# Kernel optimization log

Measured on AMD Instinct MI355X. Metric: run time of the kernel, lower is better.

The kernel has to match this reference:

```python
import jax, jax.numpy as jnp
import numpy as np

B, T, E, H, HS, L, V = 128, 256, 384, 6, 64, 6, 78
FF = 4 * E  # 1536


def layer_norm(x, g, b, eps=1e-5):
    mu = jnp.mean(x, axis=-1, keepdims=True)
    var = jnp.mean((x - mu) ** 2, axis=-1, keepdims=True)
    return (x - mu) * jax.lax.rsqrt(var + eps) * g + b


def setup_inputs() -> dict:
    key = jax.random.key(0)
    ks = jax.random.split(key, 20)
    s = 0.02
    return {
        "context": jax.random.randint(ks[0], (B, T), 0, V),
        "tok_emb": jax.random.normal(ks[1], (V, E)) * s,
        "pos_emb": jax.random.normal(ks[2], (T, E)) * s,
        "ln1_g": jnp.ones((L, E)), "ln1_b": jnp.zeros((L, E)),
        "w_qkv": jax.random.normal(ks[3], (L, H, E, 3 * HS)) * s,  # per-head qkv, no bias
        "w_proj": jax.random.normal(ks[4], (L, E, E)) * s,
        "b_proj": jnp.zeros((L, E)),
        "ln2_g": jnp.ones((L, E)), "ln2_b": jnp.zeros((L, E)),
        "w1": jax.random.normal(ks[5], (L, E, FF)) * s, "b1": jnp.zeros((L, FF)),
        "w2": jax.random.normal(ks[6], (L, FF, E)) * s, "b2": jnp.zeros((L, E)),
        "lnf_g": jnp.ones((E,)), "lnf_b": jnp.zeros((E,)),
        "w_head": jax.random.normal(ks[7], (E, V)) * s, "b_head": jnp.zeros((V,)),
    }


def reference(context, tok_emb, pos_emb, ln1_g, ln1_b, w_qkv, w_proj, b_proj,
              ln2_g, ln2_b, w1, b1, w2, b2, lnf_g, lnf_b, w_head, b_head):
    x = tok_emb[context] + pos_emb[None, :, :]            # [B,T,E]
    causal = jnp.tril(jnp.ones((T, T), dtype=bool))       # lower-tri mask
    scale = HS ** (-0.5)
    for l in range(L):
        # multi-head attention (pre-LN), per-head qkv projection, no bias
        xn = layer_norm(x, ln1_g[l], ln1_b[l])
        qkv = jnp.einsum('bte,hef->bthf', xn, w_qkv[l])   # [B,T,H,3*HS]
        q, k, v = jnp.split(qkv, 3, axis=-1)              # each [B,T,H,HS]
        scores = jnp.einsum('bthd,bshd->bhts', q, k) * scale
        scores = jnp.where(causal, scores, -jnp.inf)
        att = jax.nn.softmax(scores, axis=-1)             # [B,H,T,T]
        o = jnp.einsum('bhts,bshd->bthd', att, v).reshape(B, T, E)
        x = x + o @ w_proj[l] + b_proj[l]
        # feed-forward (pre-LN)
        xn2 = layer_norm(x, ln2_g[l], ln2_b[l])
        x = x + jax.nn.relu(xn2 @ w1[l] + b1[l]) @ w2[l] + b2[l]
    x = layer_norm(x, lnf_g, lnf_b)
    return x @ w_head + b_head                            # [B,T,V]
```

## Files before the change

### kernel.cpp

```cpp
#include <hip/hip_runtime.h>


#define Bc 128
#define Tc 256
#define Ec 384
#define Hc 6
#define HSc 64
#define Lc 6
#define Vc 78
#define FFc 1536
#define Mc (Bc * Tc)

typedef unsigned short u16;
using bf16x8 = __attribute__((ext_vector_type(8))) short;
using f32x4 = __attribute__((ext_vector_type(4))) float;

__device__ __forceinline__ float b2f(u16 u) {
    union { float f; unsigned int i; } x;
    x.i = ((unsigned int)u) << 16;
    return x.f;
}
__device__ __forceinline__ u16 f2b(float f) {
    union { float f; unsigned int u; } x;
    x.f = f;
    unsigned int r = x.u + 0x7fffu + ((x.u >> 16) & 1u);
    return (u16)(r >> 16);
}

__device__ __forceinline__ void gload_lds16(const u16* g, u16* l) {
    __builtin_amdgcn_global_load_lds(
        (const __attribute__((address_space(1))) unsigned int*)g,
        (__attribute__((address_space(3))) unsigned int*)l, 16, 0, 0);
}

__global__ __launch_bounds__(256) void poison_kernel(
    float* __restrict__ out, int n, float val) {
    int i = blockIdx.x * 256 + threadIdx.x;
    if (i < n) out[i] = val;
}

__global__ __launch_bounds__(256) void trans_qkv_kernel(
    const float* __restrict__ in, u16* __restrict__ out) {
    int i = blockIdx.x * 256 + threadIdx.x;
    if (i >= Lc * Hc * Ec * 192) return;
    int f = i % 192;
    int r = i / 192;
    int e = r % Ec; r /= Ec;
    int h = r % Hc;
    int l = r / Hc;
    out[((size_t)l * 1152 + h * 192 + f) * Ec + e] = f2b(in[i]);
}
__global__ __launch_bounds__(256) void trans_w_kernel(
    const float* __restrict__ in, u16* __restrict__ out, int K, int N) {
    int i = blockIdx.x * 256 + threadIdx.x;
    if (i >= Lc * K * N) return;
    int n = i % N;
    int r = i / N;
    int k = r % K;
    int l = r / K;
    out[((size_t)l * N + n) * K + k] = f2b(in[i]);
}
__global__ __launch_bounds__(256) void trans_head_kernel(
    const float* __restrict__ in, u16* __restrict__ out) {
    int i = blockIdx.x * 256 + threadIdx.x;
    if (i >= Ec * Vc) return;
    int v = i % Vc, e = i / Vc;
    out[(size_t)v * Ec + e] = f2b(in[i]);
}

__global__ __launch_bounds__(256) void embed_kernel(
    const int* __restrict__ ctx, const float* __restrict__ tok,
    const float* __restrict__ pos, float* __restrict__ x) {
    int i = blockIdx.x * 256 + threadIdx.x;
    if (i >= Mc * Ec) return;
    int e = i % Ec, bt = i / Ec, t = bt % Tc;
    x[i] = tok[ctx[bt] * Ec + e] + pos[t * Ec + e];
}

__global__ __launch_bounds__(256) void ln_kernel(
    const float* __restrict__ X, u16* __restrict__ Y,
    const float* __restrict__ g, const float* __restrict__ b, int nrows) {
    int row = blockIdx.x * 4 + (threadIdx.x >> 6);
    int lane = threadIdx.x & 63;
    if (row >= nrows) return;
    const float* xr = X + (size_t)row * Ec;
    float v[6];
    float s = 0.f;
#pragma unroll
    for (int i = 0; i < 6; ++i) { v[i] = xr[lane + 64 * i]; s += v[i]; }
#pragma unroll
    for (int off = 32; off >= 1; off >>= 1) s += __shfl_xor(s, off, 64);
    float mean = s * (1.0f / Ec);
    float s2 = 0.f;
#pragma unroll
    for (int i = 0; i < 6; ++i) { float d = v[i] - mean; s2 += d * d; }
#pragma unroll
    for (int off = 32; off >= 1; off >>= 1) s2 += __shfl_xor(s2, off, 64);
    float rstd = rsqrtf(s2 * (1.0f / Ec) + 1e-5f);
    u16* yr = Y + (size_t)row * Ec;
#pragma unroll
    for (int i = 0; i < 6; ++i) {
        int e = lane + 64 * i;
        yr[e] = f2b((v[i] - mean) * rstd * g[e] + b[e]);
    }
}

template <bool RELU, bool RESID, bool OUTBF16, bool VECEPI>
__global__ __launch_bounds__(256) void mfma_gemm(
    const u16* __restrict__ A, const u16* __restrict__ Wt,
    const float* __restrict__ bias, const float* R, void* C,
    int K, int ldC, int NV) {
    constexpr bool SWAP = VECEPI && !OUTBF16;
    __shared__ __align__(16) u16 smem[128 * 128];
    u16(*As)[64] = (u16(*)[64])smem;
    u16(*Bs)[64] = (u16(*)[64])(smem + 128 * 64);
    int tid = threadIdx.x;

    int nwg = gridDim.x * gridDim.y;
    int bid = blockIdx.y * gridDim.x + blockIdx.x;
    int q = nwg >> 3, r = nwg & 7;
    int xcd = bid & 7, idx = bid >> 3;
    int swz = (xcd < r ? xcd * (q + 1) : r * (q + 1) + (xcd - r) * q) + idx;
    int bx = swz % gridDim.x, by = swz / gridDim.x;
    int m0 = by * 128, n0 = bx * 128;

    int w = tid >> 6, lane = tid & 63;
    int wm = (w >> 1) * 64, wn = (w & 1) * 64;
    int r16 = lane & 15, quad = lane >> 4;

    int lrow = lane >> 3;
    int scol = ((lane & 7) ^ lrow) * 8;
    const u16* ap[4];
    const u16* bp[4];
#pragma unroll
    for (int j = 0; j < 4; ++j) {
        int row = (w * 4 + j) * 8 + lrow;
        ap[j] = A + (size_t)(m0 + row) * K + scol;
        bp[j] = Wt + (size_t)(n0 + row) * K + scol;
    }

    f32x4 acc[4][4] = {};

    for (int k0 = 0; k0 < K; k0 += 64) {
        __syncthreads();
#pragma unroll
        for (int j = 0; j < 4; ++j) {
            gload_lds16(ap[j], &As[(w * 4 + j) * 8][0]);
            gload_lds16(bp[j], &Bs[(w * 4 + j) * 8][0]);
            ap[j] += 64;
            bp[j] += 64;
        }
        __syncthreads();
#pragma unroll
        for (int kk = 0; kk < 2; ++kk) {
            int csw = ((kk * 4 + quad) ^ (r16 & 7)) * 8;
            bf16x8 af[4], bf[4];
#pragma unroll
            for (int i = 0; i < 4; ++i) {
                af[i] = *reinterpret_cast<const bf16x8*>(
                    &As[wm + i * 16 + r16][csw]);
                bf[i] = *reinterpret_cast<const bf16x8*>(
                    &Bs[wn + i * 16 + r16][csw]);
            }
#pragma unroll
            for (int mi = 0; mi < 4; ++mi)
#pragma unroll
                for (int ni = 0; ni < 4; ++ni) {
                    if (SWAP)
                        acc[mi][ni] = __builtin_amdgcn_mfma_f32_16x16x32_bf16(
                            bf[ni], af[mi], acc[mi][ni], 0, 0, 0);
                    else
                        acc[mi][ni] = __builtin_amdgcn_mfma_f32_16x16x32_bf16(
                            af[mi], bf[ni], acc[mi][ni], 0, 0, 0);
                }
        }
    }

    if (VECEPI && OUTBF16) {
        float bv[4];
#pragma unroll
        for (int ni = 0; ni < 4; ++ni)
            bv[ni] = bias ? bias[n0 + wn + ni * 16 + r16] : 0.f;
        __syncthreads();
#pragma unroll
        for (int mi = 0; mi < 4; ++mi)
#pragma unroll
            for (int ni = 0; ni < 4; ++ni)
#pragma unroll
                for (int reg = 0; reg < 4; ++reg) {
                    int row = wm + mi * 16 + quad * 4 + reg;
                    int col = wn + ni * 16 + r16;
                    float v = acc[mi][ni][reg] + bv[ni];
                    if (RELU) v = fmaxf(v, 0.f);
                    int pc = (col >> 3) ^ (row & 15);
                    smem[row * 128 + pc * 8 + (col & 7)] = f2b(v);
                }
        __syncthreads();
        u16* cp = (u16*)C;
#pragma unroll
        for (int i = 0; i < 4; ++i) {
            int row = (tid >> 3) + 32 * i;
#pragma unroll
            for (int h = 0; h < 2; ++h) {
                int lc = (tid & 7) + 8 * h;
                int pc = lc ^ (row & 15);
                bf16x8 val = *reinterpret_cast<const bf16x8*>(
                    &smem[row * 128 + pc * 8]);
                *reinterpret_cast<bf16x8*>(
                    &cp[(size_t)(m0 + row) * ldC + n0 + lc * 8]) = val;
            }
        }
    } else if (VECEPI) {
        float* cp = (float*)C;
        f32x4 bv4[4];
#pragma unroll
        for (int ni = 0; ni < 4; ++ni) {
            int gn = n0 + wn + ni * 16 + quad * 4;
            if (bias)
                bv4[ni] = *reinterpret_cast<const f32x4*>(&bias[gn]);
            else
                bv4[ni] = f32x4{0.f, 0.f, 0.f, 0.f};
        }
#pragma unroll
        for (int mi = 0; mi < 4; ++mi) {
            int gm = m0 + wm + mi * 16 + r16;
#pragma unroll
            for (int ni = 0; ni < 4; ++ni) {
                int gn = n0 + wn + ni * 16 + quad * 4;
                size_t goff = (size_t)gm * ldC + gn;
                f32x4 v = acc[mi][ni] + bv4[ni];
                if (RELU) {
#pragma unroll
                    for (int e = 0; e < 4; ++e) v[e] = fmaxf(v[e], 0.f);
                }
                if (RESID) v += *reinterpret_cast<const f32x4*>(&R[goff]);
                *reinterpret_cast<f32x4*>(&cp[goff]) = v;
            }
        }
    } else {
#pragma unroll
        for (int mi = 0; mi < 4; ++mi)
#pragma unroll
            for (int ni = 0; ni < 4; ++ni) {
                int gn = n0 + wn + ni * 16 + r16;
                if (gn >= NV) continue;
                float bvs = bias ? bias[gn] : 0.f;
#pragma unroll
                for (int reg = 0; reg < 4; ++reg) {
                    int gm = m0 + wm + mi * 16 + quad * 4 + reg;
                    float v = acc[mi][ni][reg] + bvs;
                    if (RESID) v += R[(size_t)gm * ldC + gn];
                    if (RELU) v = fmaxf(v, 0.f);
                    if (OUTBF16)
                        ((u16*)C)[(size_t)gm * ldC + gn] = f2b(v);
                    else
                        ((float*)C)[(size_t)gm * ldC + gn] = v;
                }
            }
    }
}

__global__ __launch_bounds__(256) void attn_kernel(
    const u16* __restrict__ qkv, u16* __restrict__ o) {
    __shared__ u16 Qs[64][72];
    __shared__ u16 Ks[64][72];
    __shared__ u16 Vt[64][72];
    __shared__ u16 Ps[4][16][72];
    int tid = threadIdx.x;
    int tt = blockIdx.x, h = blockIdx.y, b = blockIdx.z;
    int w = tid >> 6, lane = tid & 63;
    int r16 = lane & 15, quad = lane >> 4;
    int t0 = tt * 64;
    const u16* base = qkv + (size_t)b * Tc * 1152 + h * 192;

    int sr = tid >> 2, sd = (tid & 3) * 16;
    {
        const u16* src = base + (size_t)(t0 + sr) * 1152 + sd;
        *reinterpret_cast<uint4*>(&Qs[sr][sd]) =
            *reinterpret_cast<const uint4*>(src);
        *reinterpret_cast<uint4*>(&Qs[sr][sd + 8]) =
            *reinterpret_cast<const uint4*>(src + 8);
    }

    float m_run[4], l_run[4];
#pragma unroll
    for (int r = 0; r < 4; ++r) { m_run[r] = -3.0e38f; l_run[r] = 0.f; }
    f32x4 acc_o[4] = {};

    for (int st = 0; st <= tt; ++st) {
        __syncthreads();
        {
            const u16* ks = base + (size_t)(st * 64 + sr) * 1152 + 64 + sd;
            *reinterpret_cast<uint4*>(&Ks[sr][sd]) =
                *reinterpret_cast<const uint4*>(ks);
            *reinterpret_cast<uint4*>(&Ks[sr][sd + 8]) =
                *reinterpret_cast<const uint4*>(ks + 8);
            const u16* vs = base + (size_t)(st * 64 + sr) * 1152 + 128 + sd;
            u16 tv[16];
            *reinterpret_cast<uint4*>(tv) = *reinterpret_cast<const uint4*>(vs);
            *reinterpret_cast<uint4*>(tv + 8) =
                *reinterpret_cast<const uint4*>(vs + 8);
#pragma unroll
            for (int j = 0; j < 16; ++j) Vt[sd + j][sr] = tv[j];
        }
        __syncthreads();

        f32x4 acc_s[4] = {};
        bf16x8 aq0 = *reinterpret_cast<const bf16x8*>(&Qs[w * 16 + r16][quad * 8]);
        bf16x8 aq1 = *reinterpret_cast<const bf16x8*>(&Qs[w * 16 + r16][32 + quad * 8]);
#pragma unroll
        for (int ni = 0; ni < 4; ++ni) {
            bf16x8 bk0 = *reinterpret_cast<const bf16x8*>(&Ks[ni * 16 + r16][quad * 8]);
            bf16x8 bk1 = *reinterpret_cast<const bf16x8*>(&Ks[ni * 16 + r16][32 + quad * 8]);
            acc_s[ni] = __builtin_amdgcn_mfma_f32_16x16x32_bf16(aq0, bk0, acc_s[ni], 0, 0, 0);
            acc_s[ni] = __builtin_amdgcn_mfma_f32_16x16x32_bf16(aq1, bk1, acc_s[ni], 0, 0, 0);
        }

        float sc[4][4];
        float mt[4] = {-3.0e38f, -3.0e38f, -3.0e38f, -3.0e38f};
#pragma unroll
        for (int ni = 0; ni < 4; ++ni)
#pragma unroll
            for (int reg = 0; reg < 4; ++reg) {
                int col = st * 64 + ni * 16 + r16;
                int row = t0 + w * 16 + quad * 4 + reg;
                float v = (col <= row) ? acc_s[ni][reg] * 0.125f : -3.0e38f;
                sc[ni][reg] = v;
                mt[reg] = fmaxf(mt[reg], v);
            }
#pragma unroll
        for (int reg = 0; reg < 4; ++reg) {
#pragma unroll
            for (int off = 1; off <= 8; off <<= 1)
                mt[reg] = fmaxf(mt[reg], __shfl_xor(mt[reg], off, 64));
        }
        float alpha[4], lt[4];
#pragma unroll
        for (int reg = 0; reg < 4; ++reg) {
            float m_new = fmaxf(m_run[reg], mt[reg]);
            alpha[reg] = __expf(m_run[reg] - m_new);
            m_run[reg] = m_new;
            lt[reg] = 0.f;
        }
#pragma unroll
        for (int ni = 0; ni < 4; ++ni)
#pragma unroll
            for (int reg = 0; reg < 4; ++reg) {
                float p = __expf(sc[ni][reg] - m_run[reg]);
                lt[reg] += p;
                Ps[w][quad * 4 + reg][ni * 16 + r16] = f2b(p);
            }
#pragma unroll
        for (int reg = 0; reg < 4; ++reg) {
#pragma unroll
            for (int off = 1; off <= 8; off <<= 1)
                lt[reg] += __shfl_xor(lt[reg], off, 64);
            l_run[reg] = l_run[reg] * alpha[reg] + lt[reg];
        }
#pragma unroll
        for (int ni = 0; ni < 4; ++ni)
#pragma unroll
            for (int reg = 0; reg < 4; ++reg) acc_o[ni][reg] *= alpha[reg];
        __syncthreads();

        bf16x8 ap0 = *reinterpret_cast<const bf16x8*>(&Ps[w][r16][quad * 8]);
        bf16x8 ap1 = *reinterpret_cast<const bf16x8*>(&Ps[w][r16][32 + quad * 8]);
#pragma unroll
        for (int ni = 0; ni < 4; ++ni) {
            bf16x8 bv0 = *reinterpret_cast<const bf16x8*>(&Vt[ni * 16 + r16][quad * 8]);
            bf16x8 bv1 = *reinterpret_cast<const bf16x8*>(&Vt[ni * 16 + r16][32 + quad * 8]);
            acc_o[ni] = __builtin_amdgcn_mfma_f32_16x16x32_bf16(ap0, bv0, acc_o[ni], 0, 0, 0);
            acc_o[ni] = __builtin_amdgcn_mfma_f32_16x16x32_bf16(ap1, bv1, acc_o[ni], 0, 0, 0);
        }
    }

    float inv[4];
#pragma unroll
    for (int reg = 0; reg < 4; ++reg) inv[reg] = 1.0f / l_run[reg];
#pragma unroll
    for (int ni = 0; ni < 4; ++ni)
#pragma unroll
        for (int reg = 0; reg < 4; ++reg) {
            int t = t0 + w * 16 + quad * 4 + reg;
            o[((size_t)b * Tc + t) * Ec + h * 64 + ni * 16 + r16] =
                f2b(acc_o[ni][reg] * inv[reg]);
        }
}

#define GRD(n) dim3(((n) + 255) / 256)

extern "C" void kernel_launch(void* const* d_in, const int* in_sizes, int n_in,
                              void* d_out, int out_size, void* d_ws, size_t ws_size,
                              hipStream_t stream) {
    const int* ctx = (const int*)d_in[0];
    const float* tok = (const float*)d_in[1];
    const float* pos = (const float*)d_in[2];
    const float* ln1g = (const float*)d_in[3];
    const float* ln1b = (const float*)d_in[4];
    const float* wqkv = (const float*)d_in[5];
    const float* wproj = (const float*)d_in[6];
    const float* bproj = (const float*)d_in[7];
    const float* ln2g = (const float*)d_in[8];
    const float* ln2b = (const float*)d_in[9];
    const float* w1 = (const float*)d_in[10];
    const float* b1 = (const float*)d_in[11];
    const float* w2 = (const float*)d_in[12];
    const float* b2 = (const float*)d_in[13];
    const float* lnfg = (const float*)d_in[14];
    const float* lnfb = (const float*)d_in[15];
    const float* whead = (const float*)d_in[16];
    const float* bhead = (const float*)d_in[17];
    float* out = (float*)d_out;

    char* ws = (char*)d_ws;
    float* x = (float*)ws;
    size_t off = (size_t)Mc * Ec * 4;
    u16* wqkvT = (u16*)(ws + off); off += (size_t)Lc * 1152 * 384 * 2;
    u16* wprojT = (u16*)(ws + off); off += (size_t)Lc * 384 * 384 * 2;
    u16* w1T = (u16*)(ws + off); off += (size_t)Lc * 1536 * 384 * 2;
    u16* w2T = (u16*)(ws + off); off += (size_t)Lc * 384 * 1536 * 2;
    u16* wheadT = (u16*)(ws + off); off += (size_t)128 * 384 * 2;
    const size_t per_b = (size_t)Tc * (Ec + 1152 + Ec + FFc) * 2;
    if (ws_size < off + per_b) {
        poison_kernel<<<GRD(out_size), 256, 0, stream>>>(out, out_size, 200.0f);
        return;
    }
    int CB = (int)((ws_size - off) / per_b);
    if (CB > Bc) CB = Bc;
    u16* xn_c = (u16*)(ws + off);
    u16* qkv_c = xn_c + (size_t)CB * Tc * Ec;
    u16* o_c = qkv_c + (size_t)CB * Tc * 1152;
    u16* ff_c = o_c + (size_t)CB * Tc * Ec;

    trans_qkv_kernel<<<GRD(Lc * Hc * Ec * 192), 256, 0, stream>>>(wqkv, wqkvT);
    trans_w_kernel<<<GRD(Lc * Ec * Ec), 256, 0, stream>>>(wproj, wprojT, Ec, Ec);
    trans_w_kernel<<<GRD(Lc * Ec * FFc), 256, 0, stream>>>(w1, w1T, Ec, FFc);
    trans_w_kernel<<<GRD(Lc * FFc * Ec), 256, 0, stream>>>(w2, w2T, FFc, Ec);
    hipMemsetAsync(wheadT, 0, (size_t)128 * 384 * 2, stream);
    trans_head_kernel<<<GRD(Ec * Vc), 256, 0, stream>>>(whead, wheadT);

    embed_kernel<<<GRD(Mc * Ec), 256, 0, stream>>>(ctx, tok, pos, x);

    for (int l = 0; l < Lc; ++l) {
        for (int b0 = 0; b0 < Bc; b0 += CB) {
            int bcnt = (Bc - b0 < CB) ? (Bc - b0) : CB;
            int rows = bcnt * Tc;
            float* xc = x + (size_t)b0 * Tc * Ec;
            ln_kernel<<<rows / 4, 256, 0, stream>>>(
                xc, xn_c, ln1g + l * Ec, ln1b + l * Ec, rows);
            mfma_gemm<false, false, true, true><<<dim3(1152 / 128, rows / 128), 256, 0, stream>>>(
                xn_c, wqkvT + (size_t)l * 1152 * 384, nullptr, nullptr, qkv_c,
                384, 1152, 1152);
            attn_kernel<<<dim3(Tc / 64, Hc, bcnt), 256, 0, stream>>>(qkv_c, o_c);
            mfma_gemm<false, true, false, true><<<dim3(Ec / 128, rows / 128), 256, 0, stream>>>(
                o_c, wprojT + (size_t)l * 384 * 384, bproj + l * Ec, xc, xc,
                384, Ec, Ec);
            ln_kernel<<<rows / 4, 256, 0, stream>>>(
                xc, xn_c, ln2g + l * Ec, ln2b + l * Ec, rows);
            mfma_gemm<true, false, true, true><<<dim3(FFc / 128, rows / 128), 256, 0, stream>>>(
                xn_c, w1T + (size_t)l * 1536 * 384, b1 + l * FFc, nullptr, ff_c,
                384, FFc, FFc);
            mfma_gemm<false, true, false, true><<<dim3(Ec / 128, rows / 128), 256, 0, stream>>>(
                ff_c, w2T + (size_t)l * 384 * 1536, b2 + l * Ec, xc, xc,
                1536, Ec, Ec);
        }
    }
    for (int b0 = 0; b0 < Bc; b0 += CB) {
        int bcnt = (Bc - b0 < CB) ? (Bc - b0) : CB;
        int rows = bcnt * Tc;
        float* xc = x + (size_t)b0 * Tc * Ec;
        ln_kernel<<<rows / 4, 256, 0, stream>>>(xc, xn_c, lnfg, lnfb, rows);
        mfma_gemm<false, false, false, false><<<dim3(1, rows / 128), 256, 0, stream>>>(
            xn_c, wheadT, bhead, nullptr, out + (size_t)b0 * Tc * Vc,
            384, Vc, Vc);
    }
}
```

Measured before the change: 2.448 ms.

## Prefetch next K/V tile into registers in attention; vectorize embed and layernorm

Result: faster. 2.319 ms (-5.3%).

```diff
diff --git a/kernel.cpp b/kernel.cpp
--- a/kernel.cpp
+++ b/kernel.cpp
@@ -72,9 +72,11 @@
     const int* __restrict__ ctx, const float* __restrict__ tok,
     const float* __restrict__ pos, float* __restrict__ x) {
     int i = blockIdx.x * 256 + threadIdx.x;
-    if (i >= Mc * Ec) return;
-    int e = i % Ec, bt = i / Ec, t = bt % Tc;
-    x[i] = tok[ctx[bt] * Ec + e] + pos[t * Ec + e];
+    if (i >= Mc * 96) return;
+    int c4 = (i % 96) * 4, bt = i / 96, t = bt % Tc;
+    f32x4 tv = *reinterpret_cast<const f32x4*>(&tok[ctx[bt] * Ec + c4]);
+    f32x4 pv = *reinterpret_cast<const f32x4*>(&pos[t * Ec + c4]);
+    *reinterpret_cast<f32x4*>(&x[(size_t)bt * Ec + c4]) = tv + pv;
 }
 
 __global__ __launch_bounds__(256) void ln_kernel(
@@ -84,24 +86,35 @@
     int lane = threadIdx.x & 63;
     if (row >= nrows) return;
     const float* xr = X + (size_t)row * Ec;
-    float v[6];
+    float2 v[3];
     float s = 0.f;
 #pragma unroll
-    for (int i = 0; i < 6; ++i) { v[i] = xr[lane + 64 * i]; s += v[i]; }
+    for (int i = 0; i < 3; ++i) {
+        v[i] = *reinterpret_cast<const float2*>(&xr[2 * lane + 128 * i]);
+        s += v[i].x + v[i].y;
+    }
 #pragma unroll
     for (int off = 32; off >= 1; off >>= 1) s += __shfl_xor(s, off, 64);
     float mean = s * (1.0f / Ec);
     float s2 = 0.f;
 #pragma unroll
-    for (int i = 0; i < 6; ++i) { float d = v[i] - mean; s2 += d * d; }
+    for (int i = 0; i < 3; ++i) {
+        float dx = v[i].x - mean, dy = v[i].y - mean;
+        s2 += dx * dx + dy * dy;
+    }
 #pragma unroll
     for (int off = 32; off >= 1; off >>= 1) s2 += __shfl_xor(s2, off, 64);
     float rstd = rsqrtf(s2 * (1.0f / Ec) + 1e-5f);
     u16* yr = Y + (size_t)row * Ec;
 #pragma unroll
-    for (int i = 0; i < 6; ++i) {
-        int e = lane + 64 * i;
-        yr[e] = f2b((v[i] - mean) * rstd * g[e] + b[e]);
+    for (int i = 0; i < 3; ++i) {
+        int e = 2 * lane + 128 * i;
+        float2 gv = *reinterpret_cast<const float2*>(&g[e]);
+        float2 bv = *reinterpret_cast<const float2*>(&b[e]);
+        ushort2 ov;
+        ov.x = f2b((v[i].x - mean) * rstd * gv.x + bv.x);
+        ov.y = f2b((v[i].y - mean) * rstd * gv.y + bv.y);
+        *reinterpret_cast<ushort2*>(&yr[e]) = ov;
     }
 }
 
@@ -281,6 +294,19 @@
         *reinterpret_cast<uint4*>(&Qs[sr][sd + 8]) =
             *reinterpret_cast<const uint4*>(src + 8);
     }
+    __syncthreads();
+    bf16x8 aq0 = *reinterpret_cast<const bf16x8*>(&Qs[w * 16 + r16][quad * 8]);
+    bf16x8 aq1 = *reinterpret_cast<const bf16x8*>(&Qs[w * 16 + r16][32 + quad * 8]);
+
+    uint4 kr0, kr1, vr0, vr1;
+    {
+        const u16* ks = base + (size_t)sr * 1152 + 64 + sd;
+        kr0 = *reinterpret_cast<const uint4*>(ks);
+        kr1 = *reinterpret_cast<const uint4*>(ks + 8);
+        const u16* vs = base + (size_t)sr * 1152 + 128 + sd;
+        vr0 = *reinterpret_cast<const uint4*>(vs);
+        vr1 = *reinterpret_cast<const uint4*>(vs + 8);
+    }
 
     float m_run[4], l_run[4];
 #pragma unroll
@@ -290,24 +316,25 @@
     for (int st = 0; st <= tt; ++st) {
         __syncthreads();
         {
-            const u16* ks = base + (size_t)(st * 64 + sr) * 1152 + 64 + sd;
-            *reinterpret_cast<uint4*>(&Ks[sr][sd]) =
-                *reinterpret_cast<const uint4*>(ks);
-            *reinterpret_cast<uint4*>(&Ks[sr][sd + 8]) =
-                *reinterpret_cast<const uint4*>(ks + 8);
-            const u16* vs = base + (size_t)(st * 64 + sr) * 1152 + 128 + sd;
+            *reinterpret_cast<uint4*>(&Ks[sr][sd]) = kr0;
+            *reinterpret_cast<uint4*>(&Ks[sr][sd + 8]) = kr1;
             u16 tv[16];
-            *reinterpret_cast<uint4*>(tv) = *reinterpret_cast<const uint4*>(vs);
-            *reinterpret_cast<uint4*>(tv + 8) =
-                *reinterpret_cast<const uint4*>(vs + 8);
+            *reinterpret_cast<uint4*>(tv) = vr0;
+            *reinterpret_cast<uint4*>(tv + 8) = vr1;
 #pragma unroll
             for (int j = 0; j < 16; ++j) Vt[sd + j][sr] = tv[j];
         }
         __syncthreads();
+        if (st < tt) {
+            const u16* ks = base + (size_t)((st + 1) * 64 + sr) * 1152 + 64 + sd;
+            kr0 = *reinterpret_cast<const uint4*>(ks);
+            kr1 = *reinterpret_cast<const uint4*>(ks + 8);
+            const u16* vs = base + (size_t)((st + 1) * 64 + sr) * 1152 + 128 + sd;
+            vr0 = *reinterpret_cast<const uint4*>(vs);
+            vr1 = *reinterpret_cast<const uint4*>(vs + 8);
+        }
 
         f32x4 acc_s[4] = {};
-        bf16x8 aq0 = *reinterpret_cast<const bf16x8*>(&Qs[w * 16 + r16][quad * 8]);
-        bf16x8 aq1 = *reinterpret_cast<const bf16x8*>(&Qs[w * 16 + r16][32 + quad * 8]);
 #pragma unroll
         for (int ni = 0; ni < 4; ++ni) {
             bf16x8 bk0 = *reinterpret_cast<const bf16x8*>(&Ks[ni * 16 + r16][quad * 8]);
@@ -439,7 +466,7 @@
     hipMemsetAsync(wheadT, 0, (size_t)128 * 384 * 2, stream);
     trans_head_kernel<<<GRD(Ec * Vc), 256, 0, stream>>>(whead, wheadT);
 
-    embed_kernel<<<GRD(Mc * Ec), 256, 0, stream>>>(ctx, tok, pos, x);
+    embed_kernel<<<GRD(Mc * 96), 256, 0, stream>>>(ctx, tok, pos, x);
 
     for (int l = 0; l < Lc; ++l) {
         for (int b0 = 0; b0 < Bc; b0 += CB) {
```
